# Kernel optimization log

Hardware: AMD Instinct MI355X
Metric: run time of the kernel (lower is better)

## Reference

```python
import jax, jax.numpy as jnp
import numpy as np

LATENT, HID = 32, 64
NODE_FEAT, EDGE_FEAT, ENERGY_DIM, STRESS_DIM = 4, 3, 2, 9
B, N, E = 256, 200000, 1500000


def _lin(key, fan_in, fan_out):
    kw, kb = jax.random.split(key)
    s = 1.0 / np.sqrt(fan_in)
    return (jax.random.uniform(kw, (fan_in, fan_out), jnp.float32, -s, s),
            jax.random.uniform(kb, (fan_out,), jnp.float32, -s, s))


def setup_inputs() -> dict:
    key = jax.random.key(0)
    ks = jax.random.split(key, 16)
    z = jax.random.normal(ks[0], (B, LATENT), jnp.float32)
    node_emb = jax.random.normal(ks[1], (N, 2 * HID), jnp.float32)
    graph_id = jnp.sort(jax.random.randint(ks[2], (N,), 0, B))
    src = jax.random.randint(ks[3], (E,), 0, N)
    dst = jax.random.randint(ks[4], (E,), 0, N)
    lp_w, lp_b = _lin(ks[5], LATENT, 2 * HID)            # latent_proj
    nep_w, nep_b = _lin(ks[6], 2 * HID, 2 * HID)          # node_emb_proj
    nd1_w, nd1_b = _lin(ks[7], 2 * HID, HID)              # node_decoder L1
    nd2_w, nd2_b = _lin(ks[8], HID, NODE_FEAT)            # node_decoder L2
    ed1_w, ed1_b = _lin(ks[9], 4 * HID, HID)              # edge_decoder L1
    ed2_w, ed2_b = _lin(ks[10], HID, EDGE_FEAT)           # edge_decoder L2
    en1_w, en1_b = _lin(ks[11], LATENT, HID)              # energy L1
    en2_w, en2_b = _lin(ks[12], HID, ENERGY_DIM)          # energy L2
    st1_w, st1_b = _lin(ks[13], LATENT, HID)              # stress L1
    st2_w, st2_b = _lin(ks[14], HID, STRESS_DIM)          # stress L2
    return dict(z=z, node_emb=node_emb, graph_id=graph_id, src=src, dst=dst,
                lp_w=lp_w, lp_b=lp_b, nep_w=nep_w, nep_b=nep_b,
                nd1_w=nd1_w, nd1_b=nd1_b, nd2_w=nd2_w, nd2_b=nd2_b,
                ed1_w=ed1_w, ed1_b=ed1_b, ed2_w=ed2_w, ed2_b=ed2_b,
                en1_w=en1_w, en1_b=en1_b, en2_w=en2_w, en2_b=en2_b,
                st1_w=st1_w, st1_b=st1_b, st2_w=st2_w, st2_b=st2_b)


def reference(z, node_emb, graph_id, src, dst,
              lp_w, lp_b, nep_w, nep_b, nd1_w, nd1_b, nd2_w, nd2_b,
              ed1_w, ed1_b, ed2_w, ed2_b, en1_w, en1_b, en2_w, en2_b,
              st1_w, st1_b, st2_w, st2_b):
    # latent_proj + per-graph broadcast (gather replaces the Python loop)
    z_proj = jax.nn.relu(z @ lp_w + lp_b)            # [B, 2H]
    z_expanded = z_proj[graph_id]                    # [N, 2H]
    # node reconstruction (dropout is identity in eval)
    nep = jax.nn.relu(node_emb @ nep_w + nep_b)      # [N, 2H]
    h = z_expanded + nep
    recon_node = jax.nn.relu(h @ nd1_w + nd1_b) @ nd2_w + nd2_b    # [N, 4]
    # edge reconstruction: gather-concat + small MLP
    edge_input = jnp.concatenate([z_expanded[src], z_expanded[dst]], axis=1)  # [E, 4H]
    recon_edge = jax.nn.relu(edge_input @ ed1_w + ed1_b) @ ed2_w + ed2_b       # [E, 3]
    # graph-level predictors
    pred_energy = jax.nn.relu(z @ en1_w + en1_b) @ en2_w + en2_b   # [B, 2]
    pred_stress = jax.nn.relu(z @ st1_w + st1_b) @ st2_w + st2_b   # [B, 9]
    return recon_node, recon_edge, pred_energy, pred_stress
```

## Files before the change

### kernel.cpp

```cpp
#include <hip/hip_runtime.h>
#include <hip/hip_bf16.h>

#define LATENT 32
#define HID 64
#define NB 256
#define NN 200000
#define NE 1500000
#define TWOH 128

#define OUT_NODE_OFF   0
#define OUT_EDGE_OFF   (NN * 4)
#define OUT_ENERGY_OFF (OUT_EDGE_OFF + NE * 3)
#define OUT_STRESS_OFF (OUT_ENERGY_OFF + NB * 2)

#define WS_ZPROJ 0
#define WS_ZC    (WS_ZPROJ + NB*TWOH)
#define WS_P1    (WS_ZC + NB*HID)
#define WS_P2    (WS_P1 + NB*HID)
#define WS_T4    (WS_P2 + NB*HID)
#define WS_W1T   (WS_T4 + NB*NB*4)
#define WS_W2T   (WS_W1T + 8192)

typedef _Float16 half8 __attribute__((ext_vector_type(8)));
typedef _Float16 half4 __attribute__((ext_vector_type(4)));
typedef float f32x4 __attribute__((ext_vector_type(4)));
typedef int i32x2 __attribute__((ext_vector_type(2)));
typedef int i32x4 __attribute__((ext_vector_type(4)));

#define WTILES 12500
#define TPW 2
#define NODE_BLK 782
#define EDGE_BLK 733

__global__ void precompute_kernel(
    const float* __restrict__ z,
    const float* __restrict__ lp_w, const float* __restrict__ lp_b,
    const float* __restrict__ nd1_w,
    const float* __restrict__ ed1_w,
    const float* __restrict__ en1_w, const float* __restrict__ en1_b,
    const float* __restrict__ en2_w, const float* __restrict__ en2_b,
    const float* __restrict__ st1_w, const float* __restrict__ st1_b,
    const float* __restrict__ st2_w, const float* __restrict__ st2_b,
    const float* __restrict__ nep_w,
    float* __restrict__ z_proj, float* __restrict__ zc,
    float* __restrict__ P1, float* __restrict__ P2,
    _Float16* __restrict__ w1s, _Float16* __restrict__ w2s,
    float* __restrict__ out_energy, float* __restrict__ out_stress)
{
    const int t = threadIdx.x;

    if (blockIdx.x >= NB) {
        const int i = (blockIdx.x - NB) * 256 + t;
        if (i < TWOH * TWOH) {
            const int ch = i >> 7, k = i & 127;
            const int dst = ch * TWOH + (((k >> 3) ^ (ch & 7)) << 3) + (k & 7);
            w1s[dst] = (_Float16)nep_w[k * TWOH + ch];
        }
        if (i < HID * TWOH) {
            const int ch = i >> 7, k = i & 127;
            const int dst = ch * TWOH + (((k >> 3) ^ (ch & 7)) << 3) + (k & 7);
            w2s[dst] = (_Float16)nd1_w[k * HID + ch];
        }
        return;
    }

    const int b = blockIdx.x;
    __shared__ float zrow[LATENT];
    __shared__ float zp[TWOH];
    __shared__ float h_en[HID];
    __shared__ float h_st[HID];

    if (t < LATENT) zrow[t] = z[b * LATENT + t];
    __syncthreads();

    if (t < TWOH) {
        float a = lp_b[t];
        #pragma unroll
        for (int k = 0; k < LATENT; ++k)
            a = fmaf(zrow[k], lp_w[k * TWOH + t], a);
        a = fmaxf(a, 0.f);
        zp[t] = a;
        z_proj[b * TWOH + t] = a;
    }
    if (t < HID) {
        float ae = en1_b[t];
        float as = st1_b[t];
        #pragma unroll
        for (int k = 0; k < LATENT; ++k) {
            ae = fmaf(zrow[k], en1_w[k * HID + t], ae);
            as = fmaf(zrow[k], st1_w[k * HID + t], as);
        }
        h_en[t] = fmaxf(ae, 0.f);
        h_st[t] = fmaxf(as, 0.f);
    }
    __syncthreads();

    if (t < HID) {
        float a = 0.f, p1 = 0.f, p2 = 0.f;
        #pragma unroll 8
        for (int k = 0; k < TWOH; ++k) {
            const float zk = zp[k];
            a  = fmaf(zk, nd1_w[k * HID + t], a);
            p1 = fmaf(zk, ed1_w[k * HID + t], p1);
            p2 = fmaf(zk, ed1_w[(TWOH + k) * HID + t], p2);
        }
        zc[b * HID + t] = a;
        P1[b * HID + t] = p1;
        P2[b * HID + t] = p2;
    }
    if (t < 2) {
        float a = en2_b[t];
        #pragma unroll 8
        for (int k = 0; k < HID; ++k) a = fmaf(h_en[k], en2_w[k * 2 + t], a);
        out_energy[b * 2 + t] = a;
    }
    if (t >= 16 && t < 25) {
        const int j = t - 16;
        float a = st2_b[j];
        #pragma unroll 8
        for (int k = 0; k < HID; ++k) a = fmaf(h_st[k], st2_w[k * 9 + j], a);
        out_stress[b * 9 + j] = a;
    }
}

__global__ void edge_table_kernel(
    const float* __restrict__ P1, const float* __restrict__ P2,
    const float* __restrict__ ed1_b,
    const float* __restrict__ ed2_w, const float* __restrict__ ed2_b,
    float4* __restrict__ T4)
{
    const int gs = blockIdx.x;
    const int t  = threadIdx.x;

    __shared__ float p1s[HID];
    __shared__ float w2s_[HID * 3];
    __shared__ float b2s[3];

    if (t < HID) p1s[t] = P1[gs * HID + t] + ed1_b[t];
    if (t >= 64 && t < 64 + HID * 3) w2s_[t - 64] = ed2_w[t - 64];
    if (t < 3) b2s[t] = ed2_b[t];
    __syncthreads();

    float o0 = b2s[0], o1 = b2s[1], o2 = b2s[2];
    const f32x4* __restrict__ p2 = reinterpret_cast<const f32x4*>(&P2[t * HID]);
    #pragma unroll 4
    for (int k4 = 0; k4 < 16; ++k4) {
        const f32x4 pv = p2[k4];
        #pragma unroll
        for (int j = 0; j < 4; ++j) {
            const int k = k4 * 4 + j;
            const float h = fmaxf(p1s[k] + pv[j], 0.f);
            o0 = fmaf(h, w2s_[k * 3 + 0], o0);
            o1 = fmaf(h, w2s_[k * 3 + 1], o1);
            o2 = fmaf(h, w2s_[k * 3 + 2], o2);
        }
    }
    T4[gs * NB + t] = make_float4(o0, o1, o2, 0.f);
}

__global__ __launch_bounds__(512, 4)
void node_edge_kernel(
    const float* __restrict__ node_emb,
    const int*   __restrict__ graph_id,
    const _Float16* __restrict__ w1s,
    const float* __restrict__ nep_b,
    const _Float16* __restrict__ w2s,
    const float* __restrict__ nd1_b,
    const float* __restrict__ nd2_w, const float* __restrict__ nd2_b,
    const float* __restrict__ zc,
    const int* __restrict__ src, const int* __restrict__ dst,
    const float4* __restrict__ T4,
    float* __restrict__ out_node, float* __restrict__ out_edge)
{
    const int tid = threadIdx.x;
    const int bid = blockIdx.x;

    if (bid >= NODE_BLK) {
        const int e0 = ((bid - NODE_BLK) * 512 + tid) * 4;
        if (e0 >= NE) return;
        const int4 s4 = *reinterpret_cast<const int4*>(&src[e0]);
        const int4 d4 = *reinterpret_cast<const int4*>(&dst[e0]);
        const int ss[4] = {s4.x, s4.y, s4.z, s4.w};
        const int dd[4] = {d4.x, d4.y, d4.z, d4.w};
        float o[12];
        #pragma unroll
        for (int j = 0; j < 4; ++j) {
            const int gs = graph_id[ss[j]];
            const int gd = graph_id[dd[j]];
            const float4 tv = T4[gs * NB + gd];
            o[j * 3 + 0] = tv.x; o[j * 3 + 1] = tv.y; o[j * 3 + 2] = tv.z;
        }
        float4* outp = reinterpret_cast<float4*>(&out_edge[(size_t)e0 * 3]);
        outp[0] = make_float4(o[0], o[1], o[2],  o[3]);
        outp[1] = make_float4(o[4], o[5], o[6],  o[7]);
        outp[2] = make_float4(o[8], o[9], o[10], o[11]);
        return;
    }

    __shared__ _Float16 w1L[TWOH * TWOH];
    __shared__ _Float16 w2L[HID * TWOH];
    __shared__ float    b1L[TWOH];
    __shared__ float    b2L[HID];
    __shared__ float    w3L[HID * 4];

    {
        const uint4* g1 = reinterpret_cast<const uint4*>(w1s);
        uint4* l1 = reinterpret_cast<uint4*>(w1L);
        #pragma unroll
        for (int i = 0; i < 4; ++i) l1[tid + 512 * i] = g1[tid + 512 * i];
        const uint4* g2 = reinterpret_cast<const uint4*>(w2s);
        uint4* l2 = reinterpret_cast<uint4*>(w2L);
        #pragma unroll
        for (int i = 0; i < 2; ++i) l2[tid + 512 * i] = g2[tid + 512 * i];
        if (tid < TWOH)    b1L[tid] = nep_b[tid];
        if (tid < HID)     b2L[tid] = nd1_b[tid];
        if (tid < HID * 4) w3L[tid] = nd2_w[tid];
    }
    __syncthreads();

    const int wv   = tid >> 6;
    const int lane = tid & 63;
    const int lrow = lane & 15;
    const int kg   = lane >> 4;
    const int hi   = kg >> 1;
    const int srcA = lrow | ((kg & 1) << 5);
    const int srcB = srcA | 16;

    #pragma unroll
    for (int tt = 0; tt < TPW; ++tt) {
        const int tile = (bid * 8 + wv) * TPW + tt;
        if (tile >= WTILES) break;
        const size_t nb16 = (size_t)tile * 16;
        const int node = (int)nb16 + lrow;

        const int g = graph_id[node];
        f32x4 zv[4];
        #pragma unroll
        for (int c2 = 0; c2 < 4; ++c2)
            zv[c2] = *reinterpret_cast<const f32x4*>(
                &zc[(size_t)g * HID + c2 * 16 + kg * 4]);

        f32x4 acc1[8];
        #pragma unroll
        for (int cht = 0; cht < 8; ++cht)
            acc1[cht] = *reinterpret_cast<const f32x4*>(&b1L[cht * 16 + kg * 4]);

        #pragma unroll
        for (int kb = 0; kb < 4; ++kb) {
            const float* ep = node_emb + (size_t)node * TWOH + kb * 32 + kg * 8;
            const f32x4 u = *reinterpret_cast<const f32x4*>(ep);
            const f32x4 v = *reinterpret_cast<const f32x4*>(ep + 4);
            half8 h;
            h[0] = (_Float16)u[0]; h[1] = (_Float16)u[1];
            h[2] = (_Float16)u[2]; h[3] = (_Float16)u[3];
            h[4] = (_Float16)v[0]; h[5] = (_Float16)v[1];
            h[6] = (_Float16)v[2]; h[7] = (_Float16)v[3];
            const int koff = (((kb * 4 + kg) ^ (lrow & 7)) << 3);
            #pragma unroll
            for (int cht = 0; cht < 8; ++cht) {
                const half8 w = *reinterpret_cast<const half8*>(
                    &w1L[(cht * 16 + lrow) * TWOH + koff]);
                acc1[cht] = __builtin_amdgcn_mfma_f32_16x16x32_f16(
                    w, h, acc1[cht], 0, 0, 0);
            }
        }

        half4 vv[8];
        #pragma unroll
        for (int cht = 0; cht < 8; ++cht) {
            half4 hv;
            #pragma unroll
            for (int j = 0; j < 4; ++j)
                hv[j] = (_Float16)fmaxf(acc1[cht][j], 0.f);
            vv[cht] = hv;
        }

        f32x4 acc2[4];
        #pragma unroll
        for (int c2 = 0; c2 < 4; ++c2)
            acc2[c2] = *reinterpret_cast<const f32x4*>(&b2L[c2 * 16 + kg * 4])
                       + zv[c2];

        #pragma unroll
        for (int kb = 0; kb < 4; ++kb) {
            const i32x2 a0 = __builtin_bit_cast(i32x2, vv[2 * kb]);
            const i32x2 a1 = __builtin_bit_cast(i32x2, vv[2 * kb + 1]);
            const int A0x = __shfl(a0.x, srcA, 64), A0y = __shfl(a0.y, srcA, 64);
            const int A1x = __shfl(a1.x, srcA, 64), A1y = __shfl(a1.y, srcA, 64);
            const int B0x = __shfl(a0.x, srcB, 64), B0y = __shfl(a0.y, srcB, 64);
            const int B1x = __shfl(a1.x, srcB, 64), B1y = __shfl(a1.y, srcB, 64);
            i32x4 wp;
            wp.x = hi ? A1x : A0x;  wp.y = hi ? A1y : A0y;
            wp.z = hi ? B1x : B0x;  wp.w = hi ? B1y : B0y;
            const half8 nB = __builtin_bit_cast(half8, wp);

            const int koff = (((kb * 4 + kg) ^ (lrow & 7)) << 3);
            #pragma unroll
            for (int c2 = 0; c2 < 4; ++c2) {
                const half8 w = *reinterpret_cast<const half8*>(
                    &w2L[(c2 * 16 + lrow) * TWOH + koff]);
                acc2[c2] = __builtin_amdgcn_mfma_f32_16x16x32_f16(
                    w, nB, acc2[c2], 0, 0, 0);
            }
        }

        f32x4 p = {0.f, 0.f, 0.f, 0.f};
        #pragma unroll
        for (int c2 = 0; c2 < 4; ++c2) {
            #pragma unroll
            for (int r = 0; r < 4; ++r) {
                const float tval = fmaxf(acc2[c2][r], 0.f);
                const f32x4 w3v = *reinterpret_cast<const f32x4*>(
                    &w3L[(c2 * 16 + kg * 4 + r) * 4]);
                p += tval * w3v;
            }
        }
        #pragma unroll
        for (int j = 0; j < 4; ++j) {
            p[j] += __shfl_xor(p[j], 16, 64);
            p[j] += __shfl_xor(p[j], 32, 64);
        }
        if (kg == 0) {
            const f32x4 b3 = *reinterpret_cast<const f32x4*>(&nd2_b[0]);
            *reinterpret_cast<f32x4*>(&out_node[(size_t)node * 4]) = p + b3;
        }
    }
}

extern "C" void kernel_launch(void* const* d_in, const int* in_sizes, int n_in,
                              void* d_out, int out_size, void* d_ws, size_t ws_size,
                              hipStream_t stream)
{
    const float* z        = (const float*)d_in[0];
    const float* node_emb = (const float*)d_in[1];
    const int*   graph_id = (const int*)  d_in[2];
    const int*   src      = (const int*)  d_in[3];
    const int*   dst      = (const int*)  d_in[4];
    const float* lp_w  = (const float*)d_in[5];
    const float* lp_b  = (const float*)d_in[6];
    const float* nep_w = (const float*)d_in[7];
    const float* nep_b = (const float*)d_in[8];
    const float* nd1_w = (const float*)d_in[9];
    const float* nd1_b = (const float*)d_in[10];
    const float* nd2_w = (const float*)d_in[11];
    const float* nd2_b = (const float*)d_in[12];
    const float* ed1_w = (const float*)d_in[13];
    const float* ed1_b = (const float*)d_in[14];
    const float* ed2_w = (const float*)d_in[15];
    const float* ed2_b = (const float*)d_in[16];
    const float* en1_w = (const float*)d_in[17];
    const float* en1_b = (const float*)d_in[18];
    const float* en2_w = (const float*)d_in[19];
    const float* en2_b = (const float*)d_in[20];
    const float* st1_w = (const float*)d_in[21];
    const float* st1_b = (const float*)d_in[22];
    const float* st2_w = (const float*)d_in[23];
    const float* st2_b = (const float*)d_in[24];

    float* out = (float*)d_out;
    float* out_node   = out + OUT_NODE_OFF;
    float* out_edge   = out + OUT_EDGE_OFF;
    float* out_energy = out + OUT_ENERGY_OFF;
    float* out_stress = out + OUT_STRESS_OFF;

    float* ws     = (float*)d_ws;
    float* z_proj = ws + WS_ZPROJ;
    float* zc     = ws + WS_ZC;
    float* P1     = ws + WS_P1;
    float* P2     = ws + WS_P2;
    float4* T4    = (float4*)(ws + WS_T4);
    _Float16* w1s = (_Float16*)(ws + WS_W1T);
    _Float16* w2s = (_Float16*)(ws + WS_W2T);

    precompute_kernel<<<NB + 64, 256, 0, stream>>>(
        z, lp_w, lp_b, nd1_w, ed1_w,
        en1_w, en1_b, en2_w, en2_b, st1_w, st1_b, st2_w, st2_b, nep_w,
        z_proj, zc, P1, P2, w1s, w2s, out_energy, out_stress);

    edge_table_kernel<<<NB, NB, 0, stream>>>(P1, P2, ed1_b, ed2_w, ed2_b, T4);

    node_edge_kernel<<<NODE_BLK + EDGE_BLK, 512, 0, stream>>>(
        node_emb, graph_id, w1s, nep_b, w2s, nd1_b, nd2_w, nd2_b, zc,
        src, dst, T4, out_node, out_edge);
}
```

Before: 255.0 us.

## Make node-edge kernel persistent with double-buffered tile loads and fused edge loop

Launches one fixed grid of 512 blocks in place of separate node and edge block ranges. Each wave handles up to four strided node tiles, issuing the next tile's node_emb loads before computing the current one so global loads overlap the MFMA work. The same blocks then run a grid-stride edge lookup loop, and s_setprio raises wave priority around the MFMA sections. This cuts the number of workgroups and the repeated shared-memory weight staging, at the cost of higher register pressure and fewer waves available to hide latency.

```diff
diff --git a/kernel.cpp b/kernel.cpp
--- a/kernel.cpp
+++ b/kernel.cpp
@@ -28,9 +28,8 @@
 typedef int i32x4 __attribute__((ext_vector_type(4)));
 
 #define WTILES 12500
-#define TPW 2
-#define NODE_BLK 782
-#define EDGE_BLK 733
+#define NODE_BLK 512
+#define WGS 4096
 
 __global__ void precompute_kernel(
     const float* __restrict__ z,
@@ -158,6 +157,107 @@
     T4[gs * NB + t] = make_float4(o0, o1, o2, 0.f);
 }
 
+#define LOAD_TILE(U_, V_, G_, TILE_) do {                                     \
+    const int node_ = (TILE_) * 16 + lrow;                                    \
+    const float* ep_ = node_emb + (size_t)node_ * TWOH + kg * 8;              \
+    _Pragma("unroll")                                                         \
+    for (int kb = 0; kb < 4; ++kb) {                                          \
+        U_[kb] = *reinterpret_cast<const f32x4*>(ep_ + kb * 32);              \
+        V_[kb] = *reinterpret_cast<const f32x4*>(ep_ + kb * 32 + 4);          \
+    }                                                                         \
+    G_ = graph_id[node_];                                                     \
+} while (0)
+
+#define COMPUTE_TILE(U_, V_, G_, TILE_) do {                                  \
+    const int node_ = (TILE_) * 16 + lrow;                                    \
+    f32x4 zv_[4];                                                             \
+    _Pragma("unroll")                                                         \
+    for (int c2 = 0; c2 < 4; ++c2)                                            \
+        zv_[c2] = *reinterpret_cast<const f32x4*>(                            \
+            &zc[(size_t)(G_) * HID + c2 * 16 + kg * 4]);                      \
+    f32x4 acc1_[8];                                                           \
+    _Pragma("unroll")                                                         \
+    for (int cht = 0; cht < 8; ++cht)                                         \
+        acc1_[cht] = *reinterpret_cast<const f32x4*>(&b1L[cht * 16 + kg * 4]);\
+    __builtin_amdgcn_s_setprio(1);                                            \
+    _Pragma("unroll")                                                         \
+    for (int kb = 0; kb < 4; ++kb) {                                          \
+        half8 h_;                                                             \
+        h_[0] = (_Float16)U_[kb][0]; h_[1] = (_Float16)U_[kb][1];             \
+        h_[2] = (_Float16)U_[kb][2]; h_[3] = (_Float16)U_[kb][3];             \
+        h_[4] = (_Float16)V_[kb][0]; h_[5] = (_Float16)V_[kb][1];             \
+        h_[6] = (_Float16)V_[kb][2]; h_[7] = (_Float16)V_[kb][3];             \
+        const int koff_ = (((kb * 4 + kg) ^ (lrow & 7)) << 3);                \
+        _Pragma("unroll")                                                     \
+        for (int cht = 0; cht < 8; ++cht) {                                   \
+            const half8 w_ = *reinterpret_cast<const half8*>(                 \
+                &w1L[(cht * 16 + lrow) * TWOH + koff_]);                      \
+            acc1_[cht] = __builtin_amdgcn_mfma_f32_16x16x32_f16(              \
+                w_, h_, acc1_[cht], 0, 0, 0);                                 \
+        }                                                                     \
+    }                                                                         \
+    __builtin_amdgcn_s_setprio(0);                                            \
+    half4 vv_[8];                                                             \
+    _Pragma("unroll")                                                         \
+    for (int cht = 0; cht < 8; ++cht) {                                       \
+        _Pragma("unroll")                                                     \
+        for (int j = 0; j < 4; ++j)                                           \
+            vv_[cht][j] = (_Float16)fmaxf(acc1_[cht][j], 0.f);                \
+    }                                                                         \
+    f32x4 acc2_[4];                                                           \
+    _Pragma("unroll")                                                         \
+    for (int c2 = 0; c2 < 4; ++c2)                                            \
+        acc2_[c2] = *reinterpret_cast<const f32x4*>(&b2L[c2 * 16 + kg * 4])   \
+                    + zv_[c2];                                                \
+    __builtin_amdgcn_s_setprio(1);                                            \
+    _Pragma("unroll")                                                         \
+    for (int kb = 0; kb < 4; ++kb) {                                          \
+        const i32x2 a0_ = __builtin_bit_cast(i32x2, vv_[2 * kb]);             \
+        const i32x2 a1_ = __builtin_bit_cast(i32x2, vv_[2 * kb + 1]);         \
+        const int A0x_ = __shfl(a0_.x, srcA, 64);                             \
+        const int A0y_ = __shfl(a0_.y, srcA, 64);                             \
+        const int A1x_ = __shfl(a1_.x, srcA, 64);                             \
+        const int A1y_ = __shfl(a1_.y, srcA, 64);                             \
+        const int B0x_ = __shfl(a0_.x, srcB, 64);                             \
+        const int B0y_ = __shfl(a0_.y, srcB, 64);                             \
+        const int B1x_ = __shfl(a1_.x, srcB, 64);                             \
+        const int B1y_ = __shfl(a1_.y, srcB, 64);                             \
+        i32x4 wp_;                                                            \
+        wp_.x = hi ? A1x_ : A0x_;  wp_.y = hi ? A1y_ : A0y_;                  \
+        wp_.z = hi ? B1x_ : B0x_;  wp_.w = hi ? B1y_ : B0y_;                  \
+        const half8 nB_ = __builtin_bit_cast(half8, wp_);                     \
+        const int koff_ = (((kb * 4 + kg) ^ (lrow & 7)) << 3);                \
+        _Pragma("unroll")                                                     \
+        for (int c2 = 0; c2 < 4; ++c2) {                                      \
+            const half8 w_ = *reinterpret_cast<const half8*>(                 \
+                &w2L[(c2 * 16 + lrow) * TWOH + koff_]);                       \
+            acc2_[c2] = __builtin_amdgcn_mfma_f32_16x16x32_f16(               \
+                w_, nB_, acc2_[c2], 0, 0, 0);                                 \
+        }                                                                     \
+    }                                                                         \
+    __builtin_amdgcn_s_setprio(0);                                            \
+    f32x4 p_ = {0.f, 0.f, 0.f, 0.f};                                          \
+    _Pragma("unroll")                                                         \
+    for (int c2 = 0; c2 < 4; ++c2) {                                          \
+        _Pragma("unroll")                                                     \
+        for (int r = 0; r < 4; ++r) {                                         \
+            const float tval_ = fmaxf(acc2_[c2][r], 0.f);                     \
+            const f32x4 w3v_ = *reinterpret_cast<const f32x4*>(               \
+                &w3L[(c2 * 16 + kg * 4 + r) * 4]);                            \
+            p_ += tval_ * w3v_;                                               \
+        }                                                                     \
+    }                                                                         \
+    _Pragma("unroll")                                                         \
+    for (int j = 0; j < 4; ++j) {                                             \
+        p_[j] += __shfl_xor(p_[j], 16, 64);                                   \
+        p_[j] += __shfl_xor(p_[j], 32, 64);                                   \
+    }                                                                         \
+    if (kg == 0) {                                                            \
+        const f32x4 b3_ = *reinterpret_cast<const f32x4*>(&nd2_b[0]);         \
+        *reinterpret_cast<f32x4*>(&out_node[(size_t)node_ * 4]) = p_ + b3_;   \
+    }                                                                         \
+} while (0)
+
 __global__ __launch_bounds__(512, 4)
 void node_edge_kernel(
     const float* __restrict__ node_emb,
@@ -175,28 +275,6 @@
     const int tid = threadIdx.x;
     const int bid = blockIdx.x;
 
-    if (bid >= NODE_BLK) {
-        const int e0 = ((bid - NODE_BLK) * 512 + tid) * 4;
-        if (e0 >= NE) return;
-        const int4 s4 = *reinterpret_cast<const int4*>(&src[e0]);
-        const int4 d4 = *reinterpret_cast<const int4*>(&dst[e0]);
-        const int ss[4] = {s4.x, s4.y, s4.z, s4.w};
-        const int dd[4] = {d4.x, d4.y, d4.z, d4.w};
-        float o[12];
-        #pragma unroll
-        for (int j = 0; j < 4; ++j) {
-            const int gs = graph_id[ss[j]];
-            const int gd = graph_id[dd[j]];
-            const float4 tv = T4[gs * NB + gd];
-            o[j * 3 + 0] = tv.x; o[j * 3 + 1] = tv.y; o[j * 3 + 2] = tv.z;
-        }
-        float4* outp = reinterpret_cast<float4*>(&out_edge[(size_t)e0 * 3]);
-        outp[0] = make_float4(o[0], o[1], o[2],  o[3]);
-        outp[1] = make_float4(o[4], o[5], o[6],  o[7]);
-        outp[2] = make_float4(o[8], o[9], o[10], o[11]);
-        return;
-    }
-
     __shared__ _Float16 w1L[TWOH * TWOH];
     __shared__ _Float16 w2L[HID * TWOH];
     __shared__ float    b1L[TWOH];
@@ -226,104 +304,44 @@
     const int srcA = lrow | ((kg & 1) << 5);
     const int srcB = srcA | 16;
 
-    #pragma unroll
-    for (int tt = 0; tt < TPW; ++tt) {
-        const int tile = (bid * 8 + wv) * TPW + tt;
-        if (tile >= WTILES) break;
-        const size_t nb16 = (size_t)tile * 16;
-        const int node = (int)nb16 + lrow;
-
-        const int g = graph_id[node];
-        f32x4 zv[4];
-        #pragma unroll
-        for (int c2 = 0; c2 < 4; ++c2)
-            zv[c2] = *reinterpret_cast<const f32x4*>(
-                &zc[(size_t)g * HID + c2 * 16 + kg * 4]);
-
-        f32x4 acc1[8];
-        #pragma unroll
-        for (int cht = 0; cht < 8; ++cht)
-            acc1[cht] = *reinterpret_cast<const f32x4*>(&b1L[cht * 16 + kg * 4]);
-
-        #pragma unroll
-        for (int kb = 0; kb < 4; ++kb) {
-            const float* ep = node_emb + (size_t)node * TWOH + kb * 32 + kg * 8;
-            const f32x4 u = *reinterpret_cast<const f32x4*>(ep);
-            const f32x4 v = *reinterpret_cast<const f32x4*>(ep + 4);
-            half8 h;
-            h[0] = (_Float16)u[0]; h[1] = (_Float16)u[1];
-            h[2] = (_Float16)u[2]; h[3] = (_Float16)u[3];
-            h[4] = (_Float16)v[0]; h[5] = (_Float16)v[1];
-            h[6] = (_Float16)v[2]; h[7] = (_Float16)v[3];
-            const int koff = (((kb * 4 + kg) ^ (lrow & 7)) << 3);
-            #pragma unroll
-            for (int cht = 0; cht < 8; ++cht) {
-                const half8 w = *reinterpret_cast<const half8*>(
-                    &w1L[(cht * 16 + lrow) * TWOH + koff]);
-                acc1[cht] = __builtin_amdgcn_mfma_f32_16x16x32_f16(
-                    w, h, acc1[cht], 0, 0, 0);
-            }
-        }
-
-        half4 vv[8];
-        #pragma unroll
-        for (int cht = 0; cht < 8; ++cht) {
-            half4 hv;
-            #pragma unroll
-            for (int j = 0; j < 4; ++j)
-                hv[j] = (_Float16)fmaxf(acc1[cht][j], 0.f);
-            vv[cht] = hv;
-        }
-
-        f32x4 acc2[4];
-        #pragma unroll
-        for (int c2 = 0; c2 < 4; ++c2)
-            acc2[c2] = *reinterpret_cast<const f32x4*>(&b2L[c2 * 16 + kg * 4])
-                       + zv[c2];
-
-        #pragma unroll
-        for (int kb = 0; kb < 4; ++kb) {
-            const i32x2 a0 = __builtin_bit_cast(i32x2, vv[2 * kb]);
-            const i32x2 a1 = __builtin_bit_cast(i32x2, vv[2 * kb + 1]);
-            const int A0x = __shfl(a0.x, srcA, 64), A0y = __shfl(a0.y, srcA, 64);
-            const int A1x = __shfl(a1.x, srcA, 64), A1y = __shfl(a1.y, srcA, 64);
-            const int B0x = __shfl(a0.x, srcB, 64), B0y = __shfl(a0.y, srcB, 64);
-            const int B1x = __shfl(a1.x, srcB, 64), B1y = __shfl(a1.y, srcB, 64);
-            i32x4 wp;
-            wp.x = hi ? A1x : A0x;  wp.y = hi ? A1y : A0y;
-            wp.z = hi ? B1x : B0x;  wp.w = hi ? B1y : B0y;
-            const half8 nB = __builtin_bit_cast(half8, wp);
-
-            const int koff = (((kb * 4 + kg) ^ (lrow & 7)) << 3);
-            #pragma unroll
-            for (int c2 = 0; c2 < 4; ++c2) {
-                const half8 w = *reinterpret_cast<const half8*>(
-                    &w2L[(c2 * 16 + lrow) * TWOH + koff]);
-                acc2[c2] = __builtin_amdgcn_mfma_f32_16x16x32_f16(
-                    w, nB, acc2[c2], 0, 0, 0);
-            }
-        }
-
-        f32x4 p = {0.f, 0.f, 0.f, 0.f};
-        #pragma unroll
-        for (int c2 = 0; c2 < 4; ++c2) {
-            #pragma unroll
-            for (int r = 0; r < 4; ++r) {
-                const float tval = fmaxf(acc2[c2][r], 0.f);
-                const f32x4 w3v = *reinterpret_cast<const f32x4*>(
-                    &w3L[(c2 * 16 + kg * 4 + r) * 4]);
-                p += tval * w3v;
-            }
-        }
+    {
+        const int wg = bid * 8 + wv;
+        const int t0 = wg, t1 = wg + WGS, t2 = wg + 2 * WGS, t3 = wg + 3 * WGS;
+        f32x4 Ua[4], Va[4]; int Ga;
+        f32x4 Ub[4], Vb[4]; int Gb;
+
+        LOAD_TILE(Ua, Va, Ga, t0);
+        LOAD_TILE(Ub, Vb, Gb, t1);
+        COMPUTE_TILE(Ua, Va, Ga, t0);
+        LOAD_TILE(Ua, Va, Ga, t2);
+        COMPUTE_TILE(Ub, Vb, Gb, t1);
+        const bool has3 = (t3 < WTILES);
+        if (has3) {
+            LOAD_TILE(Ub, Vb, Gb, t3);
+        }
+        COMPUTE_TILE(Ua, Va, Ga, t2);
+        if (has3) {
+            COMPUTE_TILE(Ub, Vb, Gb, t3);
+        }
+    }
+
+    for (int e0 = (bid * 512 + tid) * 4; e0 < NE; e0 += NODE_BLK * 512 * 4) {
+        const int4 s4 = *reinterpret_cast<const int4*>(&src[e0]);
+        const int4 d4 = *reinterpret_cast<const int4*>(&dst[e0]);
+        const int ss[4] = {s4.x, s4.y, s4.z, s4.w};
+        const int dd[4] = {d4.x, d4.y, d4.z, d4.w};
+        float o[12];
         #pragma unroll
         for (int j = 0; j < 4; ++j) {
-            p[j] += __shfl_xor(p[j], 16, 64);
-            p[j] += __shfl_xor(p[j], 32, 64);
-        }
-        if (kg == 0) {
-            const f32x4 b3 = *reinterpret_cast<const f32x4*>(&nd2_b[0]);
-            *reinterpret_cast<f32x4*>(&out_node[(size_t)node * 4]) = p + b3;
-        }
+            const int gs = graph_id[ss[j]];
+            const int gd = graph_id[dd[j]];
+            const float4 tv = T4[gs * NB + gd];
+            o[j * 3 + 0] = tv.x; o[j * 3 + 1] = tv.y; o[j * 3 + 2] = tv.z;
+        }
+        float4* outp = reinterpret_cast<float4*>(&out_edge[(size_t)e0 * 3]);
+        outp[0] = make_float4(o[0], o[1], o[2],  o[3]);
+        outp[1] = make_float4(o[4], o[5], o[6],  o[7]);
+        outp[2] = make_float4(o[8], o[9], o[10], o[11]);
     }
 }
 
@@ -379,7 +397,7 @@
 
     edge_table_kernel<<<NB, NB, 0, stream>>>(P1, P2, ed1_b, ed2_w, ed2_b, T4);
 
-    node_edge_kernel<<<NODE_BLK + EDGE_BLK, 512, 0, stream>>>(
+    node_edge_kernel<<<NODE_BLK, 512, 0, stream>>>(
         node_emb, graph_id, w1s, nep_b, w2s, nd1_b, nd2_w, nd2_b, zc,
         src, dst, T4, out_node, out_edge);
 }
```

After: 266.5 us. 4.5% more time.

## Drop LDS weight staging; read permuted fp16 weights from global, remove shuffles

Applied to the files above, without the earlier changes.

The node MLP path stops copying the fp16 weight matrices into shared memory. Each wave now reads its MFMA weight fragments straight from global/L2. The second-layer weights are pre-permuted in the precompute kernel so the first MFMA's output layout can feed the second MFMA directly, which removes the cross-lane shuffle transpose. Blocks shrink to 256 threads with one 16-node tile per wave, and s_setprio is raised around the MFMA loops. This cuts the per-block LDS fill cost and the barrier, but adds repeated global weight reads per wave.

```diff
diff --git a/kernel.cpp b/kernel.cpp
--- a/kernel.cpp
+++ b/kernel.cpp
@@ -18,8 +18,8 @@
 #define WS_P1    (WS_ZC + NB*HID)
 #define WS_P2    (WS_P1 + NB*HID)
 #define WS_T4    (WS_P2 + NB*HID)
-#define WS_W1T   (WS_T4 + NB*NB*4)
-#define WS_W2T   (WS_W1T + 8192)
+#define WS_W1H   (WS_T4 + NB*NB*4)
+#define WS_W2P   (WS_W1H + 8192)
 
 typedef _Float16 half8 __attribute__((ext_vector_type(8)));
 typedef _Float16 half4 __attribute__((ext_vector_type(4)));
@@ -27,10 +27,8 @@
 typedef int i32x2 __attribute__((ext_vector_type(2)));
 typedef int i32x4 __attribute__((ext_vector_type(4)));
 
-#define WTILES 12500
-#define TPW 2
-#define NODE_BLK 782
-#define EDGE_BLK 733
+#define NODE_B 3125
+#define EDGE_B 1465
 
 __global__ void precompute_kernel(
     const float* __restrict__ z,
@@ -44,7 +42,7 @@
     const float* __restrict__ nep_w,
     float* __restrict__ z_proj, float* __restrict__ zc,
     float* __restrict__ P1, float* __restrict__ P2,
-    _Float16* __restrict__ w1s, _Float16* __restrict__ w2s,
+    _Float16* __restrict__ w1h, _Float16* __restrict__ w2p,
     float* __restrict__ out_energy, float* __restrict__ out_stress)
 {
     const int t = threadIdx.x;
@@ -52,14 +50,14 @@
     if (blockIdx.x >= NB) {
         const int i = (blockIdx.x - NB) * 256 + t;
         if (i < TWOH * TWOH) {
-            const int ch = i >> 7, k = i & 127;
-            const int dst = ch * TWOH + (((k >> 3) ^ (ch & 7)) << 3) + (k & 7);
-            w1s[dst] = (_Float16)nep_w[k * TWOH + ch];
+            const int ch1 = i >> 7, k = i & 127;
+            w1h[i] = (_Float16)nep_w[k * TWOH + ch1];
         }
         if (i < HID * TWOH) {
-            const int ch = i >> 7, k = i & 127;
-            const int dst = ch * TWOH + (((k >> 3) ^ (ch & 7)) << 3) + (k & 7);
-            w2s[dst] = (_Float16)nd1_w[k * HID + ch];
+            const int ch2 = i >> 7, tp = i & 127;
+            const int kbp = tp >> 5, kg = (tp >> 3) & 3, j = tp & 7;
+            const int ch = kbp * 32 + ((j >> 2) << 4) + kg * 4 + (j & 3);
+            w2p[i] = (_Float16)nd1_w[ch * HID + ch2];
         }
         return;
     }
@@ -158,13 +156,13 @@
     T4[gs * NB + t] = make_float4(o0, o1, o2, 0.f);
 }
 
-__global__ __launch_bounds__(512, 4)
+__global__ __launch_bounds__(256, 6)
 void node_edge_kernel(
     const float* __restrict__ node_emb,
     const int*   __restrict__ graph_id,
-    const _Float16* __restrict__ w1s,
+    const _Float16* __restrict__ w1h,
     const float* __restrict__ nep_b,
-    const _Float16* __restrict__ w2s,
+    const _Float16* __restrict__ w2p,
     const float* __restrict__ nd1_b,
     const float* __restrict__ nd2_w, const float* __restrict__ nd2_b,
     const float* __restrict__ zc,
@@ -175,8 +173,8 @@
     const int tid = threadIdx.x;
     const int bid = blockIdx.x;
 
-    if (bid >= NODE_BLK) {
-        const int e0 = ((bid - NODE_BLK) * 512 + tid) * 4;
+    if (bid >= NODE_B) {
+        const int e0 = ((bid - NODE_B) * 256 + tid) * 4;
         if (e0 >= NE) return;
         const int4 s4 = *reinterpret_cast<const int4*>(&src[e0]);
         const int4 d4 = *reinterpret_cast<const int4*>(&dst[e0]);
@@ -197,133 +195,91 @@
         return;
     }
 
-    __shared__ _Float16 w1L[TWOH * TWOH];
-    __shared__ _Float16 w2L[HID * TWOH];
-    __shared__ float    b1L[TWOH];
-    __shared__ float    b2L[HID];
-    __shared__ float    w3L[HID * 4];
-
-    {
-        const uint4* g1 = reinterpret_cast<const uint4*>(w1s);
-        uint4* l1 = reinterpret_cast<uint4*>(w1L);
-        #pragma unroll
-        for (int i = 0; i < 4; ++i) l1[tid + 512 * i] = g1[tid + 512 * i];
-        const uint4* g2 = reinterpret_cast<const uint4*>(w2s);
-        uint4* l2 = reinterpret_cast<uint4*>(w2L);
-        #pragma unroll
-        for (int i = 0; i < 2; ++i) l2[tid + 512 * i] = g2[tid + 512 * i];
-        if (tid < TWOH)    b1L[tid] = nep_b[tid];
-        if (tid < HID)     b2L[tid] = nd1_b[tid];
-        if (tid < HID * 4) w3L[tid] = nd2_w[tid];
-    }
-    __syncthreads();
-
     const int wv   = tid >> 6;
     const int lane = tid & 63;
     const int lrow = lane & 15;
     const int kg   = lane >> 4;
-    const int hi   = kg >> 1;
-    const int srcA = lrow | ((kg & 1) << 5);
-    const int srcB = srcA | 16;
-
-    #pragma unroll
-    for (int tt = 0; tt < TPW; ++tt) {
-        const int tile = (bid * 8 + wv) * TPW + tt;
-        if (tile >= WTILES) break;
-        const size_t nb16 = (size_t)tile * 16;
-        const int node = (int)nb16 + lrow;
-
-        const int g = graph_id[node];
-        f32x4 zv[4];
-        #pragma unroll
-        for (int c2 = 0; c2 < 4; ++c2)
-            zv[c2] = *reinterpret_cast<const f32x4*>(
-                &zc[(size_t)g * HID + c2 * 16 + kg * 4]);
-
-        f32x4 acc1[8];
-        #pragma unroll
-        for (int cht = 0; cht < 8; ++cht)
-            acc1[cht] = *reinterpret_cast<const f32x4*>(&b1L[cht * 16 + kg * 4]);
-
-        #pragma unroll
-        for (int kb = 0; kb < 4; ++kb) {
-            const float* ep = node_emb + (size_t)node * TWOH + kb * 32 + kg * 8;
-            const f32x4 u = *reinterpret_cast<const f32x4*>(ep);
-            const f32x4 v = *reinterpret_cast<const f32x4*>(ep + 4);
-            half8 h;
-            h[0] = (_Float16)u[0]; h[1] = (_Float16)u[1];
-            h[2] = (_Float16)u[2]; h[3] = (_Float16)u[3];
-            h[4] = (_Float16)v[0]; h[5] = (_Float16)v[1];
-            h[6] = (_Float16)v[2]; h[7] = (_Float16)v[3];
-            const int koff = (((kb * 4 + kg) ^ (lrow & 7)) << 3);
-            #pragma unroll
-            for (int cht = 0; cht < 8; ++cht) {
-                const half8 w = *reinterpret_cast<const half8*>(
-                    &w1L[(cht * 16 + lrow) * TWOH + koff]);
-                acc1[cht] = __builtin_amdgcn_mfma_f32_16x16x32_f16(
-                    w, h, acc1[cht], 0, 0, 0);
-            }
-        }
-
-        half4 vv[8];
+    const int tile = bid * 4 + wv;
+    const int node = tile * 16 + lrow;
+
+    const int g = graph_id[node];
+
+    f32x4 acc1[8];
+    #pragma unroll
+    for (int cht = 0; cht < 8; ++cht)
+        acc1[cht] = *reinterpret_cast<const f32x4*>(&nep_b[cht * 16 + kg * 4]);
+
+    const float* ep = node_emb + (size_t)node * TWOH + kg * 8;
+    __builtin_amdgcn_s_setprio(1);
+    #pragma unroll
+    for (int kb = 0; kb < 4; ++kb) {
+        const f32x4 u = *reinterpret_cast<const f32x4*>(ep + kb * 32);
+        const f32x4 v = *reinterpret_cast<const f32x4*>(ep + kb * 32 + 4);
+        half8 h;
+        h[0] = (_Float16)u[0]; h[1] = (_Float16)u[1];
+        h[2] = (_Float16)u[2]; h[3] = (_Float16)u[3];
+        h[4] = (_Float16)v[0]; h[5] = (_Float16)v[1];
+        h[6] = (_Float16)v[2]; h[7] = (_Float16)v[3];
         #pragma unroll
         for (int cht = 0; cht < 8; ++cht) {
-            half4 hv;
-            #pragma unroll
-            for (int j = 0; j < 4; ++j)
-                hv[j] = (_Float16)fmaxf(acc1[cht][j], 0.f);
-            vv[cht] = hv;
-        }
-
-        f32x4 acc2[4];
-        #pragma unroll
-        for (int c2 = 0; c2 < 4; ++c2)
-            acc2[c2] = *reinterpret_cast<const f32x4*>(&b2L[c2 * 16 + kg * 4])
-                       + zv[c2];
-
-        #pragma unroll
-        for (int kb = 0; kb < 4; ++kb) {
-            const i32x2 a0 = __builtin_bit_cast(i32x2, vv[2 * kb]);
-            const i32x2 a1 = __builtin_bit_cast(i32x2, vv[2 * kb + 1]);
-            const int A0x = __shfl(a0.x, srcA, 64), A0y = __shfl(a0.y, srcA, 64);
-            const int A1x = __shfl(a1.x, srcA, 64), A1y = __shfl(a1.y, srcA, 64);
-            const int B0x = __shfl(a0.x, srcB, 64), B0y = __shfl(a0.y, srcB, 64);
-            const int B1x = __shfl(a1.x, srcB, 64), B1y = __shfl(a1.y, srcB, 64);
-            i32x4 wp;
-            wp.x = hi ? A1x : A0x;  wp.y = hi ? A1y : A0y;
-            wp.z = hi ? B1x : B0x;  wp.w = hi ? B1y : B0y;
-            const half8 nB = __builtin_bit_cast(half8, wp);
-
-            const int koff = (((kb * 4 + kg) ^ (lrow & 7)) << 3);
-            #pragma unroll
-            for (int c2 = 0; c2 < 4; ++c2) {
-                const half8 w = *reinterpret_cast<const half8*>(
-                    &w2L[(c2 * 16 + lrow) * TWOH + koff]);
-                acc2[c2] = __builtin_amdgcn_mfma_f32_16x16x32_f16(
-                    w, nB, acc2[c2], 0, 0, 0);
-            }
-        }
-
-        f32x4 p = {0.f, 0.f, 0.f, 0.f};
+            const half8 w = *reinterpret_cast<const half8*>(
+                &w1h[(cht * 16 + lrow) * TWOH + kb * 32 + kg * 8]);
+            acc1[cht] = __builtin_amdgcn_mfma_f32_16x16x32_f16(
+                w, h, acc1[cht], 0, 0, 0);
+        }
+    }
+    __builtin_amdgcn_s_setprio(0);
+
+    half4 vv[8];
+    #pragma unroll
+    for (int cht = 0; cht < 8; ++cht) {
+        #pragma unroll
+        for (int j = 0; j < 4; ++j)
+            vv[cht][j] = (_Float16)fmaxf(acc1[cht][j], 0.f);
+    }
+
+    f32x4 acc2[4];
+    #pragma unroll
+    for (int c2 = 0; c2 < 4; ++c2)
+        acc2[c2] = *reinterpret_cast<const f32x4*>(&nd1_b[c2 * 16 + kg * 4])
+                 + *reinterpret_cast<const f32x4*>(&zc[(size_t)g * HID + c2 * 16 + kg * 4]);
+
+    __builtin_amdgcn_s_setprio(1);
+    #pragma unroll
+    for (int kbp = 0; kbp < 4; ++kbp) {
+        const i32x2 lo = __builtin_bit_cast(i32x2, vv[2 * kbp]);
+        const i32x2 hi = __builtin_bit_cast(i32x2, vv[2 * kbp + 1]);
+        i32x4 c; c.x = lo.x; c.y = lo.y; c.z = hi.x; c.w = hi.y;
+        const half8 nB = __builtin_bit_cast(half8, c);
         #pragma unroll
         for (int c2 = 0; c2 < 4; ++c2) {
-            #pragma unroll
-            for (int r = 0; r < 4; ++r) {
-                const float tval = fmaxf(acc2[c2][r], 0.f);
-                const f32x4 w3v = *reinterpret_cast<const f32x4*>(
-                    &w3L[(c2 * 16 + kg * 4 + r) * 4]);
-                p += tval * w3v;
-            }
-        }
-        #pragma unroll
-        for (int j = 0; j < 4; ++j) {
-            p[j] += __shfl_xor(p[j], 16, 64);
-            p[j] += __shfl_xor(p[j], 32, 64);
-        }
-        if (kg == 0) {
-            const f32x4 b3 = *reinterpret_cast<const f32x4*>(&nd2_b[0]);
-            *reinterpret_cast<f32x4*>(&out_node[(size_t)node * 4]) = p + b3;
-        }
+            const half8 w = *reinterpret_cast<const half8*>(
+                &w2p[(c2 * 16 + lrow) * TWOH + kbp * 32 + kg * 8]);
+            acc2[c2] = __builtin_amdgcn_mfma_f32_16x16x32_f16(
+                w, nB, acc2[c2], 0, 0, 0);
+        }
+    }
+    __builtin_amdgcn_s_setprio(0);
+
+    f32x4 p = {0.f, 0.f, 0.f, 0.f};
+    #pragma unroll
+    for (int c2 = 0; c2 < 4; ++c2) {
+        #pragma unroll
+        for (int r = 0; r < 4; ++r) {
+            const float tval = fmaxf(acc2[c2][r], 0.f);
+            const f32x4 w3v = *reinterpret_cast<const f32x4*>(
+                &nd2_w[(c2 * 16 + kg * 4 + r) * 4]);
+            p += tval * w3v;
+        }
+    }
+    #pragma unroll
+    for (int j = 0; j < 4; ++j) {
+        p[j] += __shfl_xor(p[j], 16, 64);
+        p[j] += __shfl_xor(p[j], 32, 64);
+    }
+    if (kg == 0) {
+        const f32x4 b3 = *reinterpret_cast<const f32x4*>(&nd2_b[0]);
+        *reinterpret_cast<f32x4*>(&out_node[(size_t)node * 4]) = p + b3;
     }
 }
 
@@ -369,17 +325,17 @@
     float* P1     = ws + WS_P1;
     float* P2     = ws + WS_P2;
     float4* T4    = (float4*)(ws + WS_T4);
-    _Float16* w1s = (_Float16*)(ws + WS_W1T);
-    _Float16* w2s = (_Float16*)(ws + WS_W2T);
+    _Float16* w1h = (_Float16*)(ws + WS_W1H);
+    _Float16* w2p = (_Float16*)(ws + WS_W2P);
 
     precompute_kernel<<<NB + 64, 256, 0, stream>>>(
         z, lp_w, lp_b, nd1_w, ed1_w,
         en1_w, en1_b, en2_w, en2_b, st1_w, st1_b, st2_w, st2_b, nep_w,
-        z_proj, zc, P1, P2, w1s, w2s, out_energy, out_stress);
+        z_proj, zc, P1, P2, w1h, w2p, out_energy, out_stress);
 
     edge_table_kernel<<<NB, NB, 0, stream>>>(P1, P2, ed1_b, ed2_w, ed2_b, T4);
 
-    node_edge_kernel<<<NODE_BLK + EDGE_BLK, 512, 0, stream>>>(
-        node_emb, graph_id, w1s, nep_b, w2s, nd1_b, nd2_w, nd2_b, zc,
+    node_edge_kernel<<<NODE_B + EDGE_B, 256, 0, stream>>>(
+        node_emb, graph_id, w1h, nep_b, w2p, nd1_b, nd2_w, nd2_b, zc,
         src, dst, T4, out_node, out_edge);
 }
```

Result: slower. 312.9 us (+22.7%).
